# Kernel optimization log

Measured on AMD Instinct MI355X. Metric: run time of the kernel, lower is better.

## Reference

```python
import jax, jax.numpy as jnp
import numpy as np

B, S, D = 8, 8192, 64
N_HASHES = 8
BUCKET_SIZE = 64
N_BUCKETS = S // BUCKET_SIZE  # 128
SELF_ATTN_VALUE = -5e4  # torch reformer TOKEN_SELF_ATTN_VALUE


def setup_inputs() -> dict:
    key = jax.random.key(0)
    k1, k2, k3 = jax.random.split(key, 3)
    qk = jax.random.normal(k1, (B, S, D), dtype=jnp.float32)
    v = jax.random.normal(k2, (B, S, D), dtype=jnp.float32)
    # LSH random rotations: (dim, n_hashes, n_buckets // 2), shared across batch/heads
    rotations = jax.random.normal(k3, (D, N_HASHES, N_BUCKETS // 2), dtype=jnp.float32)
    return {"qk": qk, "v": v, "rotations": rotations, "query_len": S}


def _look_one_back(x):
    # concatenate each chunk with the preceding chunk (wrapping) along the kv axis
    x_extra = jnp.concatenate([x[:, -1:], x[:, :-1]], axis=1)
    return jnp.concatenate([x, x_extra], axis=2)


def _lsh_bucketed_dots(qk, v, rotations):
    batch, seqlen, dim = qk.shape
    n_buckets = seqlen // BUCKET_SIZE
    # --- hash vectors: rotate, concat with negation, argmax -> bucket ids ---
    rotated = jnp.einsum('btf,fhi->bhti', qk, rotations)           # (B, H, S, nb/2)
    rotated = jnp.concatenate([rotated, -rotated], axis=-1)        # (B, H, S, nb)
    buckets = jnp.argmax(rotated, axis=-1)                         # (B, H, S) int
    offsets = (jnp.arange(N_HASHES) * n_buckets)[None, :, None]    # disjoint per round
    buckets = (buckets + offsets).reshape(batch, -1)               # (B, H*S)

    # --- stable bucket sort via composite key (all keys unique) ---
    ticker = jnp.arange(N_HASHES * seqlen)[None, :]                # (1, H*S)
    buckets_and_t = seqlen * buckets + (ticker % seqlen)
    sticker = jnp.argsort(buckets_and_t, axis=-1)                  # sort permutation
    undo_sort = jnp.argsort(sticker, axis=-1)                      # inverse permutation
    st = sticker % seqlen                                          # original token ids

    # --- gather tokens into bucket order ---
    sqk = jnp.take_along_axis(qk, st[..., None], axis=1)           # (B, H*S, D)
    sv = jnp.take_along_axis(v, st[..., None], axis=1)

    n_chunks = N_HASHES * n_buckets
    bq_t = st.reshape(batch, n_chunks, BUCKET_SIZE)                # (B, C, bs)
    bqk = sqk.reshape(batch, n_chunks, BUCKET_SIZE, dim)
    bv = sv.reshape(batch, n_chunks, BUCKET_SIZE, dim)

    bq = bqk
    bk = bqk / (jnp.linalg.norm(bqk, axis=-1, keepdims=True) + 1e-6)  # unit-length keys

    bk = _look_one_back(bk)       # (B, C, 2*bs, D)
    bv = _look_one_back(bv)
    bkv_t = _look_one_back(bq_t)  # (B, C, 2*bs)

    dots = jnp.einsum('buie,buje->buij', bq, bk) * (dim ** -0.5)   # (B, C, bs, 2*bs)
    self_mask = bq_t[:, :, :, None] == bkv_t[:, :, None, :]
    dots = jnp.where(self_mask, SELF_ATTN_VALUE, dots)
    return dots, undo_sort, bv


def reference(qk, v, rotations, query_len):
    batch, seqlen, dim = qk.shape
    dots, undo_sort, bv = _lsh_bucketed_dots(qk, v, rotations)
    dots_logsumexp = jax.nn.logsumexp(dots, axis=-1, keepdims=True)
    p = jnp.exp(dots - dots_logsumexp)                             # per-bucket softmax
    bo = jnp.einsum('buij,buje->buie', p, bv)                      # (B, C, bs, D)
    so = bo.reshape(batch, -1, dim)                                # (B, H*S, D)
    slogits = dots_logsumexp.reshape(batch, -1)                    # (B, H*S)
    # undo the bucket sort
    o = jnp.take_along_axis(so, undo_sort[..., None], axis=1)
    logits = jnp.take_along_axis(slogits, undo_sort, axis=1)
    o = o.reshape(batch, N_HASHES, seqlen, dim)[:, :, :query_len]
    logits = logits.reshape(batch, N_HASHES, seqlen, 1)[:, :, :query_len]
    # combine across hash rounds, weighted by per-round logsumexp
    probs = jnp.exp(logits - jax.nn.logsumexp(logits, axis=1, keepdims=True))
    out = jnp.sum(o * probs, axis=1)                               # (B, query_len, D)
    return out
```

## Files before the change

### kernel.cpp

```cpp
#include <hip/hip_runtime.h>
#include <math.h>

#define B_  8
#define S_  8192
#define D_  64
#define H_  8
#define NB_ 128
#define NC_ 1024
#define REP_CAP 65536
#define T2_ 2e-3f

typedef _Float16 f16x8 __attribute__((ext_vector_type(8)));
typedef _Float16 f16x2 __attribute__((ext_vector_type(2)));
typedef float    f32x4 __attribute__((ext_vector_type(4)));
typedef unsigned int uint_;

#define MFMA16(A, Bv, C) __builtin_amdgcn_mfma_f32_16x16x32_f16(A, Bv, C, 0, 0, 0)

__global__ __launch_bounds__(256) void prep_kernel(
    const float* __restrict__ rot, _Float16* __restrict__ rotHi,
    _Float16* __restrict__ rotLo, int* __restrict__ cnt,
    const float* __restrict__ qk, const float* __restrict__ v,
    _Float16* __restrict__ q16, _Float16* __restrict__ kn16,
    _Float16* __restrict__ v16)
{
  __shared__ float rs[64 * 64];
  const int tid = threadIdx.x;

  if (blockIdx.x < 8) {
    const int h = blockIdx.x;
    if (h == 0 && tid == 0) *cnt = 0;
#pragma unroll
    for (int it = 0; it < 16; ++it) {
      const int f = it * 4 + (tid >> 6), i = tid & 63;
      rs[f * 64 + i] = rot[f * 512 + h * 64 + i];
    }
    __syncthreads();
    const int i = tid & 63, grp = tid >> 6;
    _Float16 hi[16], lo[16];
#pragma unroll
    for (int ff = 0; ff < 16; ++ff) {
      const float x = rs[(grp * 16 + ff) * 64 + i];
      hi[ff] = (_Float16)x;
      lo[ff] = (_Float16)(x - (float)hi[ff]);
    }
    f16x8* dH = (f16x8*)(rotHi + h * 4096 + i * 64 + grp * 16);
    f16x8* dL = (f16x8*)(rotLo + h * 4096 + i * 64 + grp * 16);
    dH[0] = ((f16x8*)hi)[0]; dH[1] = ((f16x8*)hi)[1];
    dL[0] = ((f16x8*)lo)[0]; dL[1] = ((f16x8*)lo)[1];
    return;
  }

  const int gt = (blockIdx.x - 8) * 64 + (tid >> 2);
  const int qu = tid & 3;
  const size_t off = (size_t)gt * 64 + qu * 16;
  float x[16];
#pragma unroll
  for (int k = 0; k < 4; ++k) ((float4*)x)[k] = ((const float4*)(qk + off))[k];
  float ss = 0.f;
#pragma unroll
  for (int k = 0; k < 16; ++k) ss = fmaf(x[k], x[k], ss);
  ss += __shfl_xor(ss, 1); ss += __shfl_xor(ss, 2);
  const float inv = 0.125f / (sqrtf(ss) + 1e-6f);
  f16x8 qh[2], kn[2];
#pragma unroll
  for (int j = 0; j < 16; ++j) {
    qh[j >> 3][j & 7] = (_Float16)x[j];
    kn[j >> 3][j & 7] = (_Float16)(x[j] * inv);
  }
  ((f16x8*)(q16  + off))[0] = qh[0]; ((f16x8*)(q16  + off))[1] = qh[1];
  ((f16x8*)(kn16 + off))[0] = kn[0]; ((f16x8*)(kn16 + off))[1] = kn[1];
  float y[16];
#pragma unroll
  for (int k = 0; k < 4; ++k) ((float4*)y)[k] = ((const float4*)(v + off))[k];
  f16x8 vv[2];
#pragma unroll
  for (int j = 0; j < 16; ++j) vv[j >> 3][j & 7] = (_Float16)y[j];
  ((f16x8*)(v16 + off))[0] = vv[0]; ((f16x8*)(v16 + off))[1] = vv[1];
}

__global__ __launch_bounds__(256) void hash_kernel(
    const float* __restrict__ qk,
    const _Float16* __restrict__ rotHi, const _Float16* __restrict__ rotLo,
    int* __restrict__ bucket, int* __restrict__ cnt, int2* __restrict__ list)
{
  __shared__ _Float16 rH[64 * 72];
  __shared__ _Float16 rL[64 * 72];
  const int tid  = threadIdx.x;
  const int tile = blockIdx.x & 127;
  const int b    = blockIdx.x >> 7;
  const int lane = tid & 63, w = tid >> 6;
  const int m16  = lane & 15, qd = lane >> 4;

  const int t = tile * 64 + w * 16 + m16;
  f16x8 BH0, BH1, BL0, BL1;
  {
    const float* src = qk + ((size_t)b * S_ + t) * 64 + 8 * qd;
    float x[16];
    ((float4*)x)[0] = ((const float4*)src)[0];
    ((float4*)x)[1] = ((const float4*)(src + 4))[0];
    ((float4*)x)[2] = ((const float4*)(src + 32))[0];
    ((float4*)x)[3] = ((const float4*)(src + 36))[0];
#pragma unroll
    for (int j = 0; j < 8; ++j) {
      const _Float16 h0 = (_Float16)x[j];
      BH0[j] = h0; BL0[j] = (_Float16)(x[j] - (float)h0);
      const _Float16 h1 = (_Float16)x[j + 8];
      BH1[j] = h1; BL1[j] = (_Float16)(x[j + 8] - (float)h1);
    }
  }
  const int srow = tid >> 2, scol = (tid & 3) * 16;
  const uint_ qd16 = (uint_)(qd << 4);

#pragma unroll 1
  for (int h = 0; h < 8; ++h) {
    __syncthreads();
    {
      const _Float16* sH = rotHi + h * 4096 + srow * 64 + scol;
      const _Float16* sL = rotLo + h * 4096 + srow * 64 + scol;
      *(f16x8*)(rH + srow * 72 + scol)     = ((const f16x8*)sH)[0];
      *(f16x8*)(rH + srow * 72 + scol + 8) = ((const f16x8*)sH)[1];
      *(f16x8*)(rL + srow * 72 + scol)     = ((const f16x8*)sL)[0];
      *(f16x8*)(rL + srow * 72 + scol + 8) = ((const f16x8*)sL)[1];
    }
    __syncthreads();

    f32x4 acc[4];
#pragma unroll
    for (int mt = 0; mt < 4; ++mt) acc[mt] = (f32x4){0.f, 0.f, 0.f, 0.f};
#pragma unroll
    for (int mt = 0; mt < 4; ++mt) {
      const _Float16* aH = rH + (16 * mt + m16) * 72 + 8 * qd;
      const _Float16* aL = rL + (16 * mt + m16) * 72 + 8 * qd;
      const f16x8 AH0 = *(const f16x8*)aH;
      const f16x8 AH1 = *(const f16x8*)(aH + 32);
      const f16x8 AL0 = *(const f16x8*)aL;
      const f16x8 AL1 = *(const f16x8*)(aL + 32);
      acc[mt] = MFMA16(AH0, BH0, acc[mt]);
      acc[mt] = MFMA16(AH1, BH1, acc[mt]);
      acc[mt] = MFMA16(AH0, BL0, acc[mt]);
      acc[mt] = MFMA16(AH1, BL1, acc[mt]);
      acc[mt] = MFMA16(AL0, BH0, acc[mt]);
      acc[mt] = MFMA16(AL1, BH1, acc[mt]);
    }

    float v1M = -1e30f, v2M = -1e30f, v1m = 1e30f, v2m = 1e30f;
#pragma unroll
    for (int mt = 0; mt < 4; ++mt)
#pragma unroll
      for (int rg = 0; rg < 4; ++rg) {
        uint_ u = __float_as_uint(acc[mt][rg]);
        u = (u & 0xFFFFFFC0u) | qd16 | (uint_)((mt << 2) | rg);
        const float xk = __uint_as_float(u);
        v2M = __builtin_amdgcn_fmed3f(v1M, v2M, xk);
        v1M = fmaxf(v1M, xk);
        v2m = __builtin_amdgcn_fmed3f(v1m, v2m, xk);
        v1m = fminf(v1m, xk);
      }
#pragma unroll
    for (int off = 16; off <= 32; off <<= 1) {
      const float o1M = __shfl_xor(v1M, off), o2M = __shfl_xor(v2M, off);
      v2M = __builtin_amdgcn_fmed3f(v1M, o1M, fmaxf(v2M, o2M));
      v1M = fmaxf(v1M, o1M);
      const float o1m = __shfl_xor(v1m, off), o2m = __shfl_xor(v2m, off);
      v2m = __builtin_amdgcn_fmed3f(v1m, o1m, fminf(v2m, o2m));
      v1m = fminf(v1m, o1m);
    }
    if (qd == 0) {
      const uint_ cM = __float_as_uint(v1M) & 63u;
      const uint_ cm = __float_as_uint(v1m) & 63u;
      const int ixM = 16 * (int)((cM >> 2) & 3u) + 4 * (int)(cM >> 4) + (int)(cM & 3u);
      const int ixm = 16 * (int)((cm >> 2) & 3u) + 4 * (int)(cm >> 4) + (int)(cm & 3u);
      const int bkt = (v1M >= -v1m) ? ixM : 64 + ixm;
      bucket[((size_t)(b * 8 + h)) * S_ + t] = bkt;
      const bool flag = ((v1M - v2M) < T2_) | ((v2m - v1m) < T2_) |
                        (fabsf(v1M + v1m) < T2_);
      if (flag) {
        const int s = atomicAdd(cnt, 1);
        if (s < REP_CAP) list[s] = make_int2(b * 8 + h, t);
      }
    }
  }
}

__global__ __launch_bounds__(256) void repair_kernel(
    const float* __restrict__ qk, const float* __restrict__ rot,
    const int* __restrict__ cnt, const int2* __restrict__ list,
    int* __restrict__ bucket)
{
  const int n = min(*cnt, REP_CAP);
  const int lane = threadIdx.x & 63;
  const int wid  = (blockIdx.x * 256 + threadIdx.x) >> 6;
  const int nw   = gridDim.x * 4;
  for (int idx = wid; idx < n; idx += nw) {
    const int bh = list[idx].x, t = list[idx].y;
    const int b = bh >> 3, hh = bh & 7;
    const float* qrow = qk + ((size_t)b * S_ + t) * D_;
    const float* rcol = rot + hh * 64 + lane;
    double acc = 0.0;
#pragma unroll 8
    for (int f = 0; f < 64; ++f)
      acc = fma((double)qrow[f], (double)rcol[(size_t)f * 512], acc);
    double vM = acc; int iM = lane;
    double vm = acc; int im = lane;
#pragma unroll
    for (int off = 32; off >= 1; off >>= 1) {
      const double voM = __shfl_xor(vM, off); const int ioM = __shfl_xor(iM, off);
      if (voM > vM || (voM == vM && ioM < iM)) { vM = voM; iM = ioM; }
      const double vom = __shfl_xor(vm, off); const int iom = __shfl_xor(im, off);
      if (vom < vm || (vom == vm && iom < im)) { vm = vom; im = iom; }
    }
    if (lane == 0) {
      const int bkt = (vM >= -vm) ? iM : 64 + im;
      bucket[(size_t)bh * S_ + t] = bkt;
    }
  }
}

__global__ __launch_bounds__(1024) void sort_kernel(
    const int* __restrict__ bucket, int* __restrict__ st)
{
  __shared__ uint_ hist[64 * 128];
  __shared__ unsigned short lb[S_];
  __shared__ int off[128];
  __shared__ int wtot;
  const int tid = threadIdx.x;
  const int bh  = blockIdx.x;
  const size_t base = (size_t)bh * S_;

#pragma unroll
  for (int k = 0; k < 8; ++k) hist[tid + k * 1024] = 0;
  __syncthreads();

#pragma unroll
  for (int k = 0; k < 8; ++k) {
    const int t = k * 1024 + tid;
    const int bk = bucket[base + t];
    lb[t] = (unsigned short)bk;
    const int g = t >> 6;
    atomicAdd(&hist[(g & 63) * 128 + bk], 1u << (16 * (g >> 6)));
  }
  __syncthreads();

  int s = 0;
  if (tid < 128) {
#pragma unroll
    for (int g = 0; g < 64; ++g) {
      const uint_ wv = hist[g * 128 + tid];
      s += (int)((wv & 0xFFFFu) + (wv >> 16));
    }
  }
  int x = s;
#pragma unroll
  for (int d = 1; d < 64; d <<= 1) {
    const int y = __shfl_up(x, d);
    if ((tid & 63) >= d) x += y;
  }
  if (tid == 63) wtot = x;
  __syncthreads();
  if (tid < 128) {
    if (tid >= 64) x += wtot;
    off[tid] = x - s;
  }
  __syncthreads();

  if (tid < 128) {
    uint_ run = (uint_)off[tid];
#pragma unroll
    for (int g = 0; g < 64; ++g) {
      const uint_ wv = hist[g * 128 + tid];
      hist[g * 128 + tid] = (wv & 0xFFFF0000u) | run;
      run += (wv & 0xFFFFu);
    }
#pragma unroll
    for (int g = 0; g < 64; ++g) {
      const uint_ wv = hist[g * 128 + tid];
      hist[g * 128 + tid] = (wv & 0xFFFFu) | (run << 16);
      run += (wv >> 16);
    }
  }
  __syncthreads();

  const int lane = tid & 63, wv_ = tid >> 6;
  const int b = bh >> 3, h = bh & 7;
  const size_t stb = (size_t)b * (H_ * S_) + (size_t)h * S_;
  const unsigned long long ltmask = (1ull << lane) - 1ull;
#pragma unroll
  for (int k = 0; k < 8; ++k) {
    const int g = wv_ * 8 + k;
    const int t = g * 64 + lane;
    const int bk = (int)lb[t];
    unsigned long long same = ~0ull;
#pragma unroll
    for (int bit = 0; bit < 7; ++bit) {
      const unsigned long long m = __ballot((bk >> bit) & 1);
      same &= ((bk >> bit) & 1) ? m : ~m;
    }
    const int rloc = __popcll(same & ltmask);
    const uint_ wd = hist[(g & 63) * 128 + bk];
    const int gbase = (int)((wd >> (16 * (g >> 6))) & 0xFFFFu);
    st[stb + gbase + rloc] = t;
  }
}

__global__ __launch_bounds__(256, 8) void attn_kernel(
    const _Float16* __restrict__ q16, const _Float16* __restrict__ kn16,
    const _Float16* __restrict__ v16, const int* __restrict__ st,
    _Float16* __restrict__ so, float* __restrict__ slog)
{
  __shared__ _Float16 smem[128 * 72];
  __shared__ __align__(16) int sIds[128];

  const int tid = threadIdx.x;
  const int c   = blockIdx.x & (NC_ - 1);
  const int b   = blockIdx.x >> 10;
  const int cm1 = (c + NC_ - 1) & (NC_ - 1);
  const size_t bst = (size_t)b * (H_ * S_);
  const size_t row0 = bst + (size_t)c * 64;
  const size_t row1 = bst + (size_t)cm1 * 64;

  const int lane = tid & 63;
  const int w    = tid >> 6;
  const int m16  = lane & 15;
  const int qd   = lane >> 4;

  if (tid < 128) sIds[tid] = (tid < 64) ? st[row0 + tid] : st[row1 + tid - 64];

  const int rid = st[row0 + 16 * w + m16];
  f16x8 q0, q1;
  {
    const _Float16* qp = q16 + ((size_t)b * S_ + rid) * 64 + 8 * qd;
    q0 = *(const f16x8*)qp;
    q1 = *(const f16x8*)(qp + 32);
  }

  const int r = tid >> 2, qu = tid & 3;
  {
    const int tokA = st[row0 + r];
    const int tokB = st[row1 + r];
    const f16x8* ska = (const f16x8*)(kn16 + ((size_t)b * S_ + tokA) * 64 + qu * 16);
    const f16x8* skb = (const f16x8*)(kn16 + ((size_t)b * S_ + tokB) * 64 + qu * 16);
    *(f16x8*)(smem + r * 72 + qu * 16)            = ska[0];
    *(f16x8*)(smem + r * 72 + qu * 16 + 8)        = ska[1];
    *(f16x8*)(smem + (64 + r) * 72 + qu * 16)     = skb[0];
    *(f16x8*)(smem + (64 + r) * 72 + qu * 16 + 8) = skb[1];
  }
  __syncthreads();

  f32x4 acc[8];
#pragma unroll
  for (int jt = 0; jt < 8; ++jt) acc[jt] = (f32x4){0.f, 0.f, 0.f, 0.f};

  __builtin_amdgcn_s_setprio(1);
#pragma unroll
  for (int jt = 0; jt < 8; ++jt) {
    const _Float16* krow = smem + (16 * jt + m16) * 72;
    const f16x8 kb0 = *(const f16x8*)(krow + 8 * qd);
    const f16x8 kb1 = *(const f16x8*)(krow + 32 + 8 * qd);
    acc[jt] = MFMA16(kb0, q0, acc[jt]);
    acc[jt] = MFMA16(kb1, q1, acc[jt]);
  }
  __builtin_amdgcn_s_setprio(0);

  float m = -1e30f;
#pragma unroll
  for (int jt = 0; jt < 8; ++jt) {
    const int4 cid = *(const int4*)(sIds + 16 * jt + 4 * qd);
    float x;
    x = acc[jt][0]; if (cid.x == rid) x = -5e4f; acc[jt][0] = x; m = fmaxf(m, x);
    x = acc[jt][1]; if (cid.y == rid) x = -5e4f; acc[jt][1] = x; m = fmaxf(m, x);
    x = acc[jt][2]; if (cid.z == rid) x = -5e4f; acc[jt][2] = x; m = fmaxf(m, x);
    x = acc[jt][3]; if (cid.w == rid) x = -5e4f; acc[jt][3] = x; m = fmaxf(m, x);
  }
  m = fmaxf(m, __shfl_xor(m, 16));
  m = fmaxf(m, __shfl_xor(m, 32));
  float sum = 0.f;
#pragma unroll
  for (int jt = 0; jt < 8; ++jt)
#pragma unroll
    for (int rg = 0; rg < 4; ++rg) {
      const float e = __expf(acc[jt][rg] - m);
      acc[jt][rg] = e;
      sum += e;
    }
  sum += __shfl_xor(sum, 16);
  sum += __shfl_xor(sum, 32);
  const float rinv = 1.f / sum;

  const int hh = c >> 7;
  const size_t hb = ((size_t)(b * 8 + hh)) * S_;
  if (qd == 0) slog[hb + rid] = m + __logf(sum);

  f16x8 pa[4];
#pragma unroll
  for (int s = 0; s < 4; ++s)
#pragma unroll
    for (int j = 0; j < 8; ++j)
      pa[s][j] = (_Float16)acc[2 * s + (j >> 2)][j & 3];

  const int c0 = 2 * r;
  const int k0 = 32 * (c0 >> 5) + 16 * ((c0 >> 2) & 1) + 4 * ((c0 >> 3) & 3) + (c0 & 3);
  const int tok0 = sIds[k0], tok1 = sIds[k0 + 1];
  f16x8 va[2], vb[2];
  {
    const f16x8* s0 = (const f16x8*)(v16 + ((size_t)b * S_ + tok0) * 64 + qu * 16);
    const f16x8* s1 = (const f16x8*)(v16 + ((size_t)b * S_ + tok1) * 64 + qu * 16);
    va[0] = s0[0]; va[1] = s0[1];
    vb[0] = s1[0]; vb[1] = s1[1];
  }
  __syncthreads();

  {
    const int swz = (qu << 3) ^ ((qu & 1) << 5);
    _Float16* dst = smem + (c0 ^ swz);
#pragma unroll
    for (int jj = 0; jj < 16; ++jj) {
      const int d = 16 * qu + jj;
      f16x2 pk; pk[0] = va[jj >> 3][jj & 7]; pk[1] = vb[jj >> 3][jj & 7];
      *(f16x2*)(dst + d * 136) = pk;
    }
  }
  __syncthreads();

  f32x4 oacc[4];
#pragma unroll
  for (int dt = 0; dt < 4; ++dt) oacc[dt] = (f32x4){0.f, 0.f, 0.f, 0.f};
  __builtin_amdgcn_s_setprio(1);
#pragma unroll
  for (int s = 0; s < 4; ++s) {
#pragma unroll
    for (int dt = 0; dt < 4; ++dt) {
      const _Float16* vp = smem + (16 * dt + m16) * 136
                         + 32 * (s ^ (dt & 1)) + 8 * (qd ^ dt);
      const f16x8 bv = *(const f16x8*)(vp);
      oacc[dt] = MFMA16(pa[s], bv, oacc[dt]);
    }
  }
  __builtin_amdgcn_s_setprio(0);

  float rin[4];
#pragma unroll
  for (int rg = 0; rg < 4; ++rg) rin[rg] = __shfl(rinv, 4 * qd + rg);

  __syncthreads();
#pragma unroll
  for (int dt = 0; dt < 4; ++dt)
#pragma unroll
    for (int rg = 0; rg < 4; ++rg)
      smem[(16 * w + 4 * qd + rg) * 72 + 16 * dt + m16] =
          (_Float16)(oacc[dt][rg] * rin[rg]);
  __syncthreads();

  {
    const int tok = sIds[r];
    const f16x8* srcp = (const f16x8*)(smem + r * 72 + qu * 16);
    const f16x8 o0 = srcp[0], o1 = srcp[1];
    f16x8* dstp = (f16x8*)(so + (hb + tok) * 64 + qu * 16);
    dstp[0] = o0; dstp[1] = o1;
  }
}

__global__ __launch_bounds__(256) void combine_kernel(
    const _Float16* __restrict__ so, const float* __restrict__ slog,
    float* __restrict__ out)
{
  const int gid = blockIdx.x * 256 + threadIdx.x;
  const int gt  = gid >> 3;
  const int oct = gid & 7;
  const int b   = gt >> 13;
  const int t   = gt & (S_ - 1);
  const size_t base8 = (size_t)(b * 8) * S_ + t;

  float l[8];
#pragma unroll
  for (int h = 0; h < 8; ++h) l[h] = slog[base8 + (size_t)h * S_];
  float m = l[0];
#pragma unroll
  for (int h = 1; h < 8; ++h) m = fmaxf(m, l[h]);
  float wv[8], W = 0.f;
#pragma unroll
  for (int h = 0; h < 8; ++h) { wv[h] = expf(l[h] - m); W += wv[h]; }
  const float iW = 1.f / W;

  float acc[8] = {0.f, 0.f, 0.f, 0.f, 0.f, 0.f, 0.f, 0.f};
#pragma unroll
  for (int h = 0; h < 8; ++h) {
    const f16x8 vv = *(const f16x8*)(so + (base8 + (size_t)h * S_) * 64 + oct * 8);
#pragma unroll
    for (int j = 0; j < 8; ++j) acc[j] = fmaf(wv[h], (float)vv[j], acc[j]);
  }
  float4 o0, o1;
  o0.x = acc[0] * iW; o0.y = acc[1] * iW; o0.z = acc[2] * iW; o0.w = acc[3] * iW;
  o1.x = acc[4] * iW; o1.y = acc[5] * iW; o1.z = acc[6] * iW; o1.w = acc[7] * iW;
  float4* dst = (float4*)(out + (size_t)gt * 64 + oct * 8);
  dst[0] = o0; dst[1] = o1;
}

extern "C" void kernel_launch(void* const* d_in, const int* in_sizes, int n_in,
                              void* d_out, int out_size, void* d_ws, size_t ws_size,
                              hipStream_t stream)
{
  const float* qk  = (const float*)d_in[0];
  const float* v   = (const float*)d_in[1];
  const float* rot = (const float*)d_in[2];
  float* out = (float*)d_out;

  char* ws = (char*)d_ws;
  const size_t MB = 1ull << 20, KB = 1024;
  int*      bucket = (int*)      (ws + 0 * MB);
  int*      st     = (int*)      (ws + 2 * MB);
  float*    slog   = (float*)    (ws + 4 * MB);
  _Float16* q16    = (_Float16*) (ws + 8 * MB);
  _Float16* kn16   = (_Float16*) (ws + 16 * MB);
  _Float16* v16    = (_Float16*) (ws + 24 * MB);
  _Float16* rotHi  = (_Float16*) (ws + 32 * MB);
  _Float16* rotLo  = (_Float16*) (ws + 32 * MB + 64 * KB);
  int*      cnt    = (int*)      (ws + 32 * MB + 128 * KB);
  int2*     list   = (int2*)     (ws + 32 * MB + 192 * KB);
  _Float16* so     = (_Float16*) (ws + 33 * MB);
  if (ws_size < 98 * MB) return;

  hipLaunchKernelGGL(prep_kernel,    dim3(8 + 1024),      dim3(256),  0, stream,
                     rot, rotHi, rotLo, cnt, qk, v, q16, kn16, v16);
  hipLaunchKernelGGL(hash_kernel,    dim3(8 * 128),       dim3(256),  0, stream,
                     qk, rotHi, rotLo, bucket, cnt, list);
  hipLaunchKernelGGL(repair_kernel,  dim3(128),           dim3(256),  0, stream,
                     qk, rot, cnt, list, bucket);
  hipLaunchKernelGGL(sort_kernel,    dim3(64),            dim3(1024), 0, stream,
                     bucket, st);
  hipLaunchKernelGGL(attn_kernel,    dim3(B_ * NC_),      dim3(256),  0, stream,
                     q16, kn16, v16, st, so, slog);
  hipLaunchKernelGGL(combine_kernel, dim3(B_ * S_ * 8 / 256), dim3(256), 0, stream,
                     so, slog, out);
}
```

Baseline: 189.8 us.

## Fuse fp16 conversion into hash kernel, transpose rotations for repair, interleave batch blocks

Moves the qk/v fp16 conversion and key normalisation out of the prep kernel and into the hash kernel, so each qk tile is read once while it is hot and the big prep launch goes away. The rotation prep now also writes a transposed fp32 copy, letting repair do contiguous float4 loads instead of strided ones. Block indexing in hash and attn now interleaves batches, which changes scheduling and cache locality across blocks. The trade-off is more work per hash-kernel block before the hash math starts.

```diff
diff --git a/kernel.cpp b/kernel.cpp
--- a/kernel.cpp
+++ b/kernel.cpp
@@ -17,80 +17,82 @@
 
 #define MFMA16(A, Bv, C) __builtin_amdgcn_mfma_f32_16x16x32_f16(A, Bv, C, 0, 0, 0)
 
-__global__ __launch_bounds__(256) void prep_kernel(
+__global__ __launch_bounds__(256) void rot_prep_kernel(
     const float* __restrict__ rot, _Float16* __restrict__ rotHi,
-    _Float16* __restrict__ rotLo, int* __restrict__ cnt,
+    _Float16* __restrict__ rotLo, float* __restrict__ rotT,
+    int* __restrict__ cnt)
+{
+  __shared__ float rs[64 * 64];
+  const int tid = threadIdx.x, h = blockIdx.x;
+  if (h == 0 && tid == 0) *cnt = 0;
+#pragma unroll
+  for (int it = 0; it < 16; ++it) {
+    const int f = it * 4 + (tid >> 6), i = tid & 63;
+    rs[f * 64 + i] = rot[f * 512 + h * 64 + i];
+  }
+  __syncthreads();
+  const int i = tid & 63, grp = tid >> 6;
+  _Float16 hi[16], lo[16];
+  float tf[16];
+#pragma unroll
+  for (int ff = 0; ff < 16; ++ff) {
+    const float x = rs[(grp * 16 + ff) * 64 + i];
+    tf[ff] = x;
+    hi[ff] = (_Float16)x;
+    lo[ff] = (_Float16)(x - (float)hi[ff]);
+  }
+  f16x8* dH = (f16x8*)(rotHi + h * 4096 + i * 64 + grp * 16);
+  f16x8* dL = (f16x8*)(rotLo + h * 4096 + i * 64 + grp * 16);
+  dH[0] = ((f16x8*)hi)[0]; dH[1] = ((f16x8*)hi)[1];
+  dL[0] = ((f16x8*)lo)[0]; dL[1] = ((f16x8*)lo)[1];
+  float4* dT = (float4*)(rotT + h * 4096 + i * 64 + grp * 16);
+#pragma unroll
+  for (int k = 0; k < 4; ++k) dT[k] = ((float4*)tf)[k];
+}
+
+__global__ __launch_bounds__(256) void hash_kernel(
     const float* __restrict__ qk, const float* __restrict__ v,
+    const _Float16* __restrict__ rotHi, const _Float16* __restrict__ rotLo,
     _Float16* __restrict__ q16, _Float16* __restrict__ kn16,
-    _Float16* __restrict__ v16)
-{
-  __shared__ float rs[64 * 64];
-  const int tid = threadIdx.x;
-
-  if (blockIdx.x < 8) {
-    const int h = blockIdx.x;
-    if (h == 0 && tid == 0) *cnt = 0;
-#pragma unroll
-    for (int it = 0; it < 16; ++it) {
-      const int f = it * 4 + (tid >> 6), i = tid & 63;
-      rs[f * 64 + i] = rot[f * 512 + h * 64 + i];
-    }
-    __syncthreads();
-    const int i = tid & 63, grp = tid >> 6;
-    _Float16 hi[16], lo[16];
-#pragma unroll
-    for (int ff = 0; ff < 16; ++ff) {
-      const float x = rs[(grp * 16 + ff) * 64 + i];
-      hi[ff] = (_Float16)x;
-      lo[ff] = (_Float16)(x - (float)hi[ff]);
-    }
-    f16x8* dH = (f16x8*)(rotHi + h * 4096 + i * 64 + grp * 16);
-    f16x8* dL = (f16x8*)(rotLo + h * 4096 + i * 64 + grp * 16);
-    dH[0] = ((f16x8*)hi)[0]; dH[1] = ((f16x8*)hi)[1];
-    dL[0] = ((f16x8*)lo)[0]; dL[1] = ((f16x8*)lo)[1];
-    return;
-  }
-
-  const int gt = (blockIdx.x - 8) * 64 + (tid >> 2);
-  const int qu = tid & 3;
-  const size_t off = (size_t)gt * 64 + qu * 16;
-  float x[16];
-#pragma unroll
-  for (int k = 0; k < 4; ++k) ((float4*)x)[k] = ((const float4*)(qk + off))[k];
-  float ss = 0.f;
-#pragma unroll
-  for (int k = 0; k < 16; ++k) ss = fmaf(x[k], x[k], ss);
-  ss += __shfl_xor(ss, 1); ss += __shfl_xor(ss, 2);
-  const float inv = 0.125f / (sqrtf(ss) + 1e-6f);
-  f16x8 qh[2], kn[2];
-#pragma unroll
-  for (int j = 0; j < 16; ++j) {
-    qh[j >> 3][j & 7] = (_Float16)x[j];
-    kn[j >> 3][j & 7] = (_Float16)(x[j] * inv);
-  }
-  ((f16x8*)(q16  + off))[0] = qh[0]; ((f16x8*)(q16  + off))[1] = qh[1];
-  ((f16x8*)(kn16 + off))[0] = kn[0]; ((f16x8*)(kn16 + off))[1] = kn[1];
-  float y[16];
-#pragma unroll
-  for (int k = 0; k < 4; ++k) ((float4*)y)[k] = ((const float4*)(v + off))[k];
-  f16x8 vv[2];
-#pragma unroll
-  for (int j = 0; j < 16; ++j) vv[j >> 3][j & 7] = (_Float16)y[j];
-  ((f16x8*)(v16 + off))[0] = vv[0]; ((f16x8*)(v16 + off))[1] = vv[1];
-}
-
-__global__ __launch_bounds__(256) void hash_kernel(
-    const float* __restrict__ qk,
-    const _Float16* __restrict__ rotHi, const _Float16* __restrict__ rotLo,
+    _Float16* __restrict__ v16,
     int* __restrict__ bucket, int* __restrict__ cnt, int2* __restrict__ list)
 {
   __shared__ _Float16 rH[64 * 72];
   __shared__ _Float16 rL[64 * 72];
   const int tid  = threadIdx.x;
-  const int tile = blockIdx.x & 127;
-  const int b    = blockIdx.x >> 7;
+  const int b    = blockIdx.x & 7;
+  const int tile = blockIdx.x >> 3;
   const int lane = tid & 63, w = tid >> 6;
   const int m16  = lane & 15, qd = lane >> 4;
+
+  {
+    const int gt = b * S_ + tile * 64 + (tid >> 2);
+    const int qu = tid & 3;
+    const size_t off = (size_t)gt * 64 + qu * 16;
+    float x[16];
+#pragma unroll
+    for (int k = 0; k < 4; ++k) ((float4*)x)[k] = ((const float4*)(qk + off))[k];
+    float ss = 0.f;
+#pragma unroll
+    for (int k = 0; k < 16; ++k) ss = fmaf(x[k], x[k], ss);
+    ss += __shfl_xor(ss, 1); ss += __shfl_xor(ss, 2);
+    const float inv = 0.125f / (sqrtf(ss) + 1e-6f);
+    f16x8 qh[2], kn[2];
+#pragma unroll
+    for (int j = 0; j < 16; ++j) {
+      qh[j >> 3][j & 7] = (_Float16)x[j];
+      kn[j >> 3][j & 7] = (_Float16)(x[j] * inv);
+    }
+    ((f16x8*)(q16  + off))[0] = qh[0]; ((f16x8*)(q16  + off))[1] = qh[1];
+    ((f16x8*)(kn16 + off))[0] = kn[0]; ((f16x8*)(kn16 + off))[1] = kn[1];
+    float y[16];
+#pragma unroll
+    for (int k = 0; k < 4; ++k) ((float4*)y)[k] = ((const float4*)(v + off))[k];
+    f16x8 vv[2];
+#pragma unroll
+    for (int j = 0; j < 16; ++j) vv[j >> 3][j & 7] = (_Float16)y[j];
+    ((f16x8*)(v16 + off))[0] = vv[0]; ((f16x8*)(v16 + off))[1] = vv[1];
+  }
 
   const int t = tile * 64 + w * 16 + m16;
   f16x8 BH0, BH1, BL0, BL1;
@@ -184,7 +186,7 @@
 }
 
 __global__ __launch_bounds__(256) void repair_kernel(
-    const float* __restrict__ qk, const float* __restrict__ rot,
+    const float* __restrict__ qk, const float* __restrict__ rotT,
     const int* __restrict__ cnt, const int2* __restrict__ list,
     int* __restrict__ bucket)
 {
@@ -196,11 +198,17 @@
     const int bh = list[idx].x, t = list[idx].y;
     const int b = bh >> 3, hh = bh & 7;
     const float* qrow = qk + ((size_t)b * S_ + t) * D_;
-    const float* rcol = rot + hh * 64 + lane;
+    const float* rcol = rotT + hh * 4096 + lane * 64;
     double acc = 0.0;
-#pragma unroll 8
-    for (int f = 0; f < 64; ++f)
-      acc = fma((double)qrow[f], (double)rcol[(size_t)f * 512], acc);
+#pragma unroll
+    for (int f0 = 0; f0 < 64; f0 += 4) {
+      const float4 rq = *(const float4*)(qrow + f0);
+      const float4 rc = *(const float4*)(rcol + f0);
+      acc = fma((double)rq.x, (double)rc.x, acc);
+      acc = fma((double)rq.y, (double)rc.y, acc);
+      acc = fma((double)rq.z, (double)rc.z, acc);
+      acc = fma((double)rq.w, (double)rc.w, acc);
+    }
     double vM = acc; int iM = lane;
     double vm = acc; int im = lane;
 #pragma unroll
@@ -312,8 +320,8 @@
   __shared__ __align__(16) int sIds[128];
 
   const int tid = threadIdx.x;
-  const int c   = blockIdx.x & (NC_ - 1);
-  const int b   = blockIdx.x >> 10;
+  const int b   = blockIdx.x & 7;
+  const int c   = blockIdx.x >> 3;
   const int cm1 = (c + NC_ - 1) & (NC_ - 1);
   const size_t bst = (size_t)b * (H_ * S_);
   const size_t row0 = bst + (size_t)c * 64;
@@ -517,19 +525,20 @@
   _Float16* rotLo  = (_Float16*) (ws + 32 * MB + 64 * KB);
   int*      cnt    = (int*)      (ws + 32 * MB + 128 * KB);
   int2*     list   = (int2*)     (ws + 32 * MB + 192 * KB);
+  float*    rotT   = (float*)    (ws + 32 * MB + 768 * KB);
   _Float16* so     = (_Float16*) (ws + 33 * MB);
   if (ws_size < 98 * MB) return;
 
-  hipLaunchKernelGGL(prep_kernel,    dim3(8 + 1024),      dim3(256),  0, stream,
-                     rot, rotHi, rotLo, cnt, qk, v, q16, kn16, v16);
-  hipLaunchKernelGGL(hash_kernel,    dim3(8 * 128),       dim3(256),  0, stream,
-                     qk, rotHi, rotLo, bucket, cnt, list);
-  hipLaunchKernelGGL(repair_kernel,  dim3(128),           dim3(256),  0, stream,
-                     qk, rot, cnt, list, bucket);
-  hipLaunchKernelGGL(sort_kernel,    dim3(64),            dim3(1024), 0, stream,
+  hipLaunchKernelGGL(rot_prep_kernel, dim3(8),         dim3(256),  0, stream,
+                     rot, rotHi, rotLo, rotT, cnt);
+  hipLaunchKernelGGL(hash_kernel,     dim3(8 * 128),   dim3(256),  0, stream,
+                     qk, v, rotHi, rotLo, q16, kn16, v16, bucket, cnt, list);
+  hipLaunchKernelGGL(repair_kernel,   dim3(128),       dim3(256),  0, stream,
+                     qk, rotT, cnt, list, bucket);
+  hipLaunchKernelGGL(sort_kernel,     dim3(64),        dim3(1024), 0, stream,
                      bucket, st);
-  hipLaunchKernelGGL(attn_kernel,    dim3(B_ * NC_),      dim3(256),  0, stream,
+  hipLaunchKernelGGL(attn_kernel,     dim3(B_ * NC_),  dim3(256),  0, stream,
                      q16, kn16, v16, st, so, slog);
-  hipLaunchKernelGGL(combine_kernel, dim3(B_ * S_ * 8 / 256), dim3(256), 0, stream,
+  hipLaunchKernelGGL(combine_kernel,  dim3(B_ * S_ * 8 / 256), dim3(256), 0, stream,
                      so, slog, out);
 }
```

Measured after the change: 180.5 us. 4.9% less time.
